# Performance work log

Measured on AMD Instinct MI355X. Metric: run time of the kernel, lower is better.

The kernel has to match this reference:

```python
import jax, jax.numpy as jnp
import numpy as np

B, T = 128, 512          # batch, sequence length (padded game length)
F_IN = 19 * 19           # flattened Go board features
H = 128                  # n_hid
P = 19 * 19 + 1          # policy classes: board points + pass


def setup_inputs() -> dict:
    key = jax.random.key(0)
    ks = jax.random.split(key, 8)
    s = 0.05  # init scale
    return {
        "states": jax.random.normal(ks[0], (B, T, F_IN), jnp.float32),
        "moves": jax.random.randint(ks[1], (B, T), 0, P, jnp.int32),
        "values": jax.random.uniform(ks[2], (B, T), jnp.float32, -1.0, 1.0),
        # LSTM layer 0: concat([x, h]) @ W0 + b0, gates [i, f, g, o]
        "W0": jax.random.normal(ks[3], (F_IN + H, 4 * H), jnp.float32) * s,
        "b0": jnp.zeros((4 * H,), jnp.float32),
        # LSTM layer 1
        "W1": jax.random.normal(ks[4], (H + H, 4 * H), jnp.float32) * s,
        "b1": jnp.zeros((4 * H,), jnp.float32),
        # policy head (size**2 + 1 logits), value head (tanh scalar)
        "Wp": jax.random.normal(ks[5], (H, P), jnp.float32) * s,
        "bp": jnp.zeros((P,), jnp.float32),
        "Wv": jax.random.normal(ks[6], (H, 1), jnp.float32) * s,
        "bv": jnp.zeros((1,), jnp.float32),
    }


def _lstm_cell(h, c, x, W, b):
    # TF LSTMCell: z = [x; h] @ W + b, forget bias 1.0
    z = jnp.concatenate([x, h], axis=-1) @ W + b
    i, f, g, o = jnp.split(z, 4, axis=-1)
    c_new = jax.nn.sigmoid(f + 1.0) * c + jax.nn.sigmoid(i) * jnp.tanh(g)
    h_new = jax.nn.sigmoid(o) * jnp.tanh(c_new)
    return h_new, c_new


def reference(states, moves, values, W0, b0, W1, b1, Wp, bp, Wv, bv):
    b = states.shape[0]
    zeros = jnp.zeros((b, H), states.dtype)

    def step(carry, x_t):
        h0, c0, h1, c1 = carry
        h0, c0 = _lstm_cell(h0, c0, x_t, W0, b0)
        h1, c1 = _lstm_cell(h1, c1, h0, W1, b1)
        return (h0, c0, h1, c1), h1

    _, hs = jax.lax.scan(step, (zeros, zeros, zeros, zeros),
                         jnp.swapaxes(states, 0, 1))  # hs: [T, B, H]
    outputs = jnp.swapaxes(hs, 0, 1)                  # [B, T, H]

    policy_logits = outputs @ Wp + bp                 # [B, T, P]
    winners = jnp.tanh(outputs @ Wv + bv)[..., 0]     # [B, T]

    mask = (values != -9.0).astype(jnp.float32)
    n_mask = mask.sum()

    logp = jax.nn.log_softmax(policy_logits, axis=-1)
    xent = -jnp.take_along_axis(logp, moves[..., None].astype(jnp.int32), axis=-1)[..., 0]
    policy_loss = (mask * xent).sum() / n_mask
    value_loss = (mask * jnp.square(winners - values)).sum() / n_mask
    acc = (moves == jnp.argmax(policy_logits, axis=-1).astype(moves.dtype)).astype(jnp.float32).mean()
    return jnp.stack([policy_loss, value_loss, acc])
```

## Files before the change

kernel.cpp:

```cpp
#include <hip/hip_runtime.h>
#include <hip/hip_bf16.h>
#include <stdint.h>


typedef short v8s __attribute__((ext_vector_type(8)));
typedef float v4f __attribute__((ext_vector_type(4)));
typedef int   v8i __attribute__((ext_vector_type(8)));

#define MFMA_B16(a,b,c) __builtin_amdgcn_mfma_f32_16x16x32_bf16((a),(b),(c),0,0,0)
#define MFMA_MX(a,b,c) \
  __builtin_amdgcn_mfma_scale_f32_16x16x128_f8f6f4((a),(b),(c),0,0,0,0x7F7F7F7F,0,0x7F7F7F7F)

#define NT     512
#define FIN    361
#define KP0    384
#define NPC    362
#define NPP    368

#define OFF_Z    ((size_t)0)
#define OFF_H1   ((size_t)83886080)
#define OFF_W0XT ((size_t)100663296)
#define OFF_WPT  ((size_t)101187584)
#define OFF_B0P  ((size_t)101281792)
#define OFF_BPP  ((size_t)101285888)
#define OFF_ACC  ((size_t)101287936)

static __device__ __forceinline__ short f2b(float f) {
  __hip_bfloat16 h = __float2bfloat16(f);
  union { __hip_bfloat16 h; short s; } cv; cv.h = h; return cv.s;
}
static __device__ __forceinline__ float b2f(unsigned int lo16) {
  union { unsigned u; float f; } cv; cv.u = lo16 << 16; return cv.f;
}
static __device__ __forceinline__ unsigned f2e4m3(float f) {
  union { float f; unsigned u; } cv; cv.f = f;
  unsigned s = (cv.u >> 31) << 7;
  float a = fabsf(f);
  a = fminf(a, 448.f);
  unsigned code;
  if (a >= 0.015625f) {
    union { float f; unsigned u; } m; m.f = a;
    unsigned u = m.u + 0x7FFFF + ((m.u >> 20) & 1);
    code = (u >> 20) - 960;
    if (code > 126u) code = 126u;
  } else {
    code = (unsigned)rintf(a * 512.f);
  }
  return s | code;
}
static __device__ __forceinline__ unsigned f2e4m3_fast(float f) {
#if __has_builtin(__builtin_amdgcn_cvt_pk_fp8_f32)
  return (unsigned)__builtin_amdgcn_cvt_pk_fp8_f32(f, f, 0, false) & 0xffu;
#else
  return f2e4m3(f);
#endif
}

static __device__ __forceinline__ void sync_lds() {
  __builtin_amdgcn_sched_barrier(0);
  asm volatile("s_waitcnt lgkmcnt(0)" ::: "memory");
  __builtin_amdgcn_s_barrier();
  __builtin_amdgcn_sched_barrier(0);
}

__global__ __launch_bounds__(256) void k_conv_weights(
    const float* __restrict__ W0, const float* __restrict__ b0,
    const float* __restrict__ Wp, const float* __restrict__ bp,
    char* __restrict__ ws) {
  int idx = blockIdx.x * 256 + threadIdx.x;
  __hip_bfloat16* W0xT = (__hip_bfloat16*)(ws + OFF_W0XT);
  __hip_bfloat16* WpT  = (__hip_bfloat16*)(ws + OFF_WPT);
  float* b0p = (float*)(ws + OFF_B0P);
  float* bpp = (float*)(ws + OFF_BPP);
  float* acc = (float*)(ws + OFF_ACC);

  if (idx < 196608) {
    int np = idx / 384, k = idx - np * 384;
    int n = (np >> 2) + 128 * (np & 3);
    float v = (k < FIN) ? W0[(size_t)k * 512 + n] : 0.f;
    W0xT[idx] = __float2bfloat16(v);
    return;
  }
  idx -= 196608;
  if (idx < 47104) {
    int p = idx >> 7, k = idx & 127;
    WpT[idx] = __float2bfloat16(p < NPC ? Wp[(size_t)k * NPC + p] : 0.f);
    return;
  }
  idx -= 47104;
  if (idx < 512) {
    int n = (idx >> 2) + 128 * (idx & 3);
    b0p[idx] = b0[n] + (((idx & 3) == 1) ? 1.0f : 0.0f);
    return;
  }
  idx -= 512;
  if (idx < NPP) { bpp[idx] = (idx < NPC) ? bp[idx] : -1e30f; return; }
  idx -= NPP;
  if (idx < 4) { acc[idx] = 0.f; return; }
}

template<int KTOT, bool AF32>
__global__ __launch_bounds__(256) void k_gemm(
    const void* __restrict__ Ap, const __hip_bfloat16* __restrict__ BT,
    const float* __restrict__ bias, __hip_bfloat16* __restrict__ C) {
  __shared__ char sm[65536];
  const int tid = threadIdx.x;
  const int l = tid & 63, wm = tid >> 6;
  const int c = l & 15, lg = l >> 4;
  const int m0 = blockIdx.x * 128;
  const int n0 = blockIdx.y * 128;
  constexpr int NS = KTOT / 64;

  uint4 ra[4], rb[4];
  float fa[32];

  auto LD = [&](int ks) {
#pragma unroll
    for (int i = 0; i < 4; i++) {
      int idx = i * 4096 + tid * 16;
      int row = idx >> 7, colb = idx & 127;
      if constexpr (AF32) {
        int r = m0 + row;
        const float* src = (const float*)Ap + ((size_t)(r & 127) * NT + (r >> 7)) * FIN;
        int kb = ks * 64 + (colb >> 1);
#pragma unroll
        for (int u = 0; u < 8; u++) {
          int kf = kb + u;
          fa[i * 8 + u] = (kf < FIN) ? src[kf] : 0.f;
        }
      } else {
        ra[i] = *(const uint4*)((const char*)Ap + ((size_t)(m0 + row) * KTOT + ks * 64) * 2 + colb);
      }
      rb[i] = *(const uint4*)((const char*)BT + ((size_t)(n0 + row) * KTOT + ks * 64) * 2 + colb);
    }
  };
  auto ST = [&](int bsel) {
#pragma unroll
    for (int i = 0; i < 4; i++) {
      int idx = i * 4096 + tid * 16;
      int row = idx >> 7, colb = idx & 127;
      int sw = colb ^ ((row & 7) << 4);
      if constexpr (AF32) {
        v8s w;
#pragma unroll
        for (int u = 0; u < 8; u++) w[u] = f2b(fa[i * 8 + u]);
        *(v8s*)(sm + bsel * 16384 + row * 128 + sw) = w;
      } else {
        *(uint4*)(sm + bsel * 16384 + row * 128 + sw) = ra[i];
      }
      *(uint4*)(sm + 32768 + bsel * 16384 + row * 128 + sw) = rb[i];
    }
  };

  v4f acc[2][8];
  v4f z4 = {0.f, 0.f, 0.f, 0.f};
#pragma unroll
  for (int mt = 0; mt < 2; mt++)
#pragma unroll
    for (int nt = 0; nt < 8; nt++) acc[mt][nt] = z4;

  LD(0); ST(0);
  __syncthreads();
  for (int ks = 0; ks < NS; ks++) {
    if (ks + 1 < NS) LD(ks + 1);
    const int bsel = ks & 1;
#pragma unroll
    for (int kk = 0; kk < 2; kk++) {
      int bir = kk * 64 + lg * 16;
      v8s af[2];
#pragma unroll
      for (int mt = 0; mt < 2; mt++) {
        int row = wm * 32 + mt * 16 + c;
        af[mt] = *(v8s*)(sm + bsel * 16384 + row * 128 + (bir ^ ((row & 7) << 4)));
      }
#pragma unroll
      for (int nt = 0; nt < 8; nt++) {
        int n = nt * 16 + c;
        v8s bf = *(v8s*)(sm + 32768 + bsel * 16384 + n * 128 + (bir ^ ((n & 7) << 4)));
#pragma unroll
        for (int mt = 0; mt < 2; mt++) acc[mt][nt] = MFMA_B16(af[mt], bf, acc[mt][nt]);
      }
    }
    if (ks + 1 < NS) ST((ks + 1) & 1);
    __syncthreads();
  }

#pragma unroll
  for (int mt = 0; mt < 2; mt++)
#pragma unroll
    for (int nt = 0; nt < 8; nt++) {
      int colp = n0 + nt * 16 + c;
      float bs = bias[colp];
#pragma unroll
      for (int j = 0; j < 4; j++) {
        int row = m0 + wm * 32 + mt * 16 + lg * 4 + j;
        C[(size_t)row * 512 + colp] = __float2bfloat16(acc[mt][nt][j] + bs);
      }
    }
}

__global__ __launch_bounds__(1024, 4) void k_scan12(
    const __hip_bfloat16* __restrict__ Z, const float* __restrict__ W0f,
    const float* __restrict__ W1f, const float* __restrict__ b1,
    __hip_bfloat16* __restrict__ h1out) {
  __shared__ char sm[8192];
  const int tid = threadIdx.x;
  const int l = tid & 63, wv = tid >> 6;
  const int c = l & 15, lg = l >> 4;
  const int role = wv >> 3, rw = wv & 7;
  const int B0 = blockIdx.x * 4;
  const int m_ = 16 * rw + c;
  const int row = 4 * lg;
  v4f z4 = {0.f, 0.f, 0.f, 0.f};
  const int wf8 = row * 128 + (((m_ >> 3) ^ row) << 3) + (m_ & 7);

  for (int e = tid * 4; e < 8192; e += 1024 * 4) *(int*)(sm + e) = 0;

  auto AFRAG = [&](int base) -> v8i {
    union { unsigned long long q[4]; v8i v; } u;
#pragma unroll
    for (int t = 0; t < 4; t++)
      u.q[t] = *(const unsigned long long*)(
          sm + base + c * 128 + ((((lg * 4 + t) ^ c) & 15) << 3));
    return u.v;
  };

  if (role == 0) {
    v8i breg[4];
#pragma unroll
    for (int g = 0; g < 4; g++) {
      int n = g * 128 + m_;
      union { unsigned long long q[4]; v8i v; } u;
#pragma unroll
      for (int t = 0; t < 4; t++) {
        unsigned long long w = 0ull;
#pragma unroll
        for (int j = 0; j < 8; j++) {
          int k = lg * 32 + t * 8 + j;
          w |= (unsigned long long)f2e4m3(W0f[(size_t)(FIN + k) * 512 + n]) << (8 * j);
        }
        u.q[t] = w;
      }
      breg[g] = u.v;
    }

    uint2 zA, zB, zC;
    auto ZLD = [&](int t) -> uint2 {
      return *(const uint2*)(Z + ((size_t)t * 128 + B0 + lg) * 512 + m_ * 4);
    };
    zA = ZLD(0); zB = ZLD(1);
    float cst = 0.f;
    __syncthreads();

    for (int s = 0; s < NT; s++) {
      v8i av = AFRAG(((s + 1) & 1) * 2048);
      v4f acc[4];
#pragma unroll
      for (int g = 0; g < 4; g++) acc[g] = z4;
#pragma unroll
      for (int g = 0; g < 4; g++) acc[g] = MFMA_MX(av, breg[g], acc[g]);
      if (s + 2 < NT) zC = ZLD(s + 2);

      float xi = acc[0][0] + b2f(zA.x & 0xffffu);
      float xf = acc[1][0] + b2f(zA.x >> 16);
      float xg = acc[2][0] + b2f(zA.y & 0xffffu);
      float xo = acc[3][0] + b2f(zA.y >> 16);
      float ei = __expf(-xi);
      float ef = __expf(-xf);
      float eg = __expf(2.f * xg);
      float eo = __expf(-xo);
      float cn = cst * __builtin_amdgcn_rcpf(1.f + ef)
               + (eg - 1.f) * __builtin_amdgcn_rcpf((1.f + ei) * (eg + 1.f));
      cst = cn;
      float ec = __expf(2.f * cn);
      float hv = (ec - 1.f) * __builtin_amdgcn_rcpf((1.f + eo) * (ec + 1.f));
      *(unsigned char*)(sm + (s & 1) * 2048 + wf8) = (unsigned char)f2e4m3_fast(hv);
      zA = zB; zB = zC;
      sync_lds();
    }
    sync_lds();
  } else {
    v8i bregH[4], bregX[4];
#pragma unroll
    for (int g = 0; g < 4; g++) {
      int n = g * 128 + m_;
      union { unsigned long long q[4]; v8i v; } uh, ux;
#pragma unroll
      for (int t = 0; t < 4; t++) {
        unsigned long long wh = 0ull, wx = 0ull;
#pragma unroll
        for (int j = 0; j < 8; j++) {
          int k = lg * 32 + t * 8 + j;
          wh |= (unsigned long long)f2e4m3(W1f[(size_t)(128 + k) * 512 + n]) << (8 * j);
          wx |= (unsigned long long)f2e4m3(W1f[(size_t)k * 512 + n]) << (8 * j);
        }
        uh.q[t] = wh; ux.q[t] = wx;
      }
      bregH[g] = uh.v; bregX[g] = ux.v;
    }
    float bq[4];
#pragma unroll
    for (int g = 0; g < 4; g++)
      bq[g] = b1[g * 128 + m_] + ((g == 1) ? 1.0f : 0.0f);
    float cst = 0.f;
    __syncthreads();
    sync_lds();

    for (int s = 1; s <= NT; s++) {
      v8i ah = AFRAG(4096 + (s & 1) * 2048);
      v8i ax = AFRAG(((s + 1) & 1) * 2048);
      v4f acc[4];
#pragma unroll
      for (int g = 0; g < 4; g++) acc[g] = (v4f){bq[g], bq[g], bq[g], bq[g]};
#pragma unroll
      for (int g = 0; g < 4; g++) acc[g] = MFMA_MX(ah, bregH[g], acc[g]);
#pragma unroll
      for (int g = 0; g < 4; g++) acc[g] = MFMA_MX(ax, bregX[g], acc[g]);

      float xi = acc[0][0], xf = acc[1][0], xg = acc[2][0], xo = acc[3][0];
      float ei = __expf(-xi);
      float ef = __expf(-xf);
      float eg = __expf(2.f * xg);
      float eo = __expf(-xo);
      float cn = cst * __builtin_amdgcn_rcpf(1.f + ef)
               + (eg - 1.f) * __builtin_amdgcn_rcpf((1.f + ei) * (eg + 1.f));
      cst = cn;
      float ec = __expf(2.f * cn);
      float hv = (ec - 1.f) * __builtin_amdgcn_rcpf((1.f + eo) * (ec + 1.f));
      *(unsigned char*)(sm + 4096 + ((s + 1) & 1) * 2048 + wf8) =
          (unsigned char)f2e4m3_fast(hv);
      union { short s; __hip_bfloat16 h; } cv; cv.s = f2b(hv);
      h1out[((size_t)(s - 1) * 128 + B0 + lg) * 128 + m_] = cv.h;
      sync_lds();
    }
  }
}

__global__ __launch_bounds__(256) void k_heads(
    const __hip_bfloat16* __restrict__ Hh, const __hip_bfloat16* __restrict__ WpT,
    const float* __restrict__ bpp, const float* __restrict__ Wv,
    const float* __restrict__ bv, const int* __restrict__ moves,
    const float* __restrict__ values, float* __restrict__ accum) {
  __shared__ char sm[110592];
  const int tid = threadIdx.x;
  const int l = tid & 63, wm = tid >> 6;
  const int c = l & 15, lg = l >> 4;
  const int r0 = blockIdx.x * 64;

#pragma unroll
  for (int i = 0; i < 4; i++) {
    int idx = i * 4096 + tid * 16;
    int row = idx >> 8, colb = idx & 255;
    uint4 v = *(const uint4*)((const char*)Hh + (size_t)r0 * 256 + idx);
    *(uint4*)(sm + row * 256 + (colb ^ ((row & 7) << 4))) = v;
  }
#pragma unroll
  for (int i = 0; i < 23; i++) {
    int idx = i * 4096 + tid * 16;
    int row = idx >> 8, colb = idx & 255;
    uint4 v = *(const uint4*)((const char*)WpT + idx);
    *(uint4*)(sm + 16384 + row * 256 + (colb ^ ((row & 7) << 4))) = v;
  }
  __syncthreads();

  v4f acc[23];
  v4f z4 = {0.f, 0.f, 0.f, 0.f};
#pragma unroll
  for (int q = 0; q < 23; q++) acc[q] = z4;
#pragma unroll
  for (int kk = 0; kk < 4; kk++) {
    int bir = kk * 64 + lg * 16;
    int ar = wm * 16 + c;
    v8s a = *(v8s*)(sm + ar * 256 + (bir ^ ((ar & 7) << 4)));
#pragma unroll
    for (int q = 0; q < 23; q++) {
      int n = q * 16 + c;
      v8s b = *(v8s*)(sm + 16384 + n * 256 + (bir ^ ((n & 7) << 4)));
      acc[q] = MFMA_B16(a, b, acc[q]);
    }
  }
  float bq[23];
#pragma unroll
  for (int q = 0; q < 23; q++) bq[q] = bpp[q * 16 + c];

  float tp = 0.f, tv = 0.f, ta = 0.f, tn = 0.f;
#pragma unroll
  for (int j = 0; j < 4; j++) {
    int rloc = lg * 4 + j;
    int r = r0 + wm * 16 + rloc;
    int t = r >> 7, b = r & 127;
    int mv = moves[(size_t)b * NT + t];
    float val = values[(size_t)b * NT + t];
    float msk = (val != -9.0f) ? 1.f : 0.f;

    float pmax = -3.0e38f;
#pragma unroll
    for (int q = 0; q < 23; q++) pmax = fmaxf(pmax, acc[q][j] + bq[q]);
#pragma unroll
    for (int d = 1; d < 16; d <<= 1) pmax = fmaxf(pmax, __shfl_xor(pmax, d, 64));
    float ps = 0.f;
#pragma unroll
    for (int q = 0; q < 23; q++) ps += __expf((acc[q][j] + bq[q]) - pmax);
#pragma unroll
    for (int d = 1; d < 16; d <<= 1) ps += __shfl_xor(ps, d, 64);
    float lse = pmax + __logf(ps);

    int qm = mv >> 4, cm = mv & 15;
    float mlv = 0.f;
#pragma unroll
    for (int q = 0; q < 23; q++) if (q == qm) mlv = acc[q][j] + bq[q];
    mlv = __shfl(mlv, (l & 48) + cm, 64);
    float xent = lse - mlv;

    float amx = -3.0e38f; int aix = 0;
#pragma unroll
    for (int q = 0; q < 23; q++) {
      float v = acc[q][j] + bq[q];
      if (v > amx) { amx = v; aix = q * 16 + c; }
    }
#pragma unroll
    for (int d = 1; d < 16; d <<= 1) {
      float ov = __shfl_xor(amx, d, 64);
      int oi = __shfl_xor(aix, d, 64);
      if (ov > amx || (ov == amx && oi < aix)) { amx = ov; aix = oi; }
    }

    float pd = 0.f;
    int vrow = wm * 16 + rloc;
#pragma unroll
    for (int i = 0; i < 8; i++) {
      int k = c * 8 + i;
      short hv = *(short*)(sm + vrow * 256 + ((k * 2) ^ ((vrow & 7) << 4)));
      pd += b2f((unsigned short)hv) * Wv[k];
    }
#pragma unroll
    for (int d = 1; d < 16; d <<= 1) pd += __shfl_xor(pd, d, 64);
    float eo = __expf(2.f * (pd + bv[0]));
    float win = (eo - 1.f) * __builtin_amdgcn_rcpf(eo + 1.f);
    float dv = win - val;

    if (c == 0) {
      tp += msk * xent;
      tv += msk * dv * dv;
      ta += (aix == mv) ? 1.f : 0.f;
      tn += msk;
    }
  }
  tp += __shfl_xor(tp, 16, 64); tp += __shfl_xor(tp, 32, 64);
  tv += __shfl_xor(tv, 16, 64); tv += __shfl_xor(tv, 32, 64);
  ta += __shfl_xor(ta, 16, 64); ta += __shfl_xor(ta, 32, 64);
  tn += __shfl_xor(tn, 16, 64); tn += __shfl_xor(tn, 32, 64);
  if (l == 0) {
    atomicAdd(accum + 0, tp);
    atomicAdd(accum + 1, tv);
    atomicAdd(accum + 2, ta);
    atomicAdd(accum + 3, tn);
  }
}

__global__ void k_final(const float* __restrict__ accum, float* __restrict__ out) {
  if (threadIdx.x == 0) {
    float nm = accum[3];
    out[0] = accum[0] / nm;
    out[1] = accum[1] / nm;
    out[2] = accum[2] / 65536.0f;
  }
}

extern "C" void kernel_launch(void* const* d_in, const int* in_sizes, int n_in,
                              void* d_out, int out_size, void* d_ws, size_t ws_size,
                              hipStream_t stream) {
  (void)in_sizes; (void)n_in; (void)out_size; (void)ws_size;
  const float* states = (const float*)d_in[0];
  const int*   moves  = (const int*)d_in[1];
  const float* values = (const float*)d_in[2];
  const float* W0 = (const float*)d_in[3];
  const float* b0 = (const float*)d_in[4];
  const float* W1 = (const float*)d_in[5];
  const float* b1 = (const float*)d_in[6];
  const float* Wp = (const float*)d_in[7];
  const float* bp = (const float*)d_in[8];
  const float* Wv = (const float*)d_in[9];
  const float* bv = (const float*)d_in[10];
  char* ws = (char*)d_ws;

  __hip_bfloat16* zbuf = (__hip_bfloat16*)(ws + OFF_Z);
  __hip_bfloat16* h1   = (__hip_bfloat16*)(ws + OFF_H1);
  __hip_bfloat16* W0xT = (__hip_bfloat16*)(ws + OFF_W0XT);
  __hip_bfloat16* WpT  = (__hip_bfloat16*)(ws + OFF_WPT);
  float* b0p = (float*)(ws + OFF_B0P);
  float* bpp = (float*)(ws + OFF_BPP);
  float* acc = (float*)(ws + OFF_ACC);

  k_conv_weights<<<956, 256, 0, stream>>>(W0, b0, Wp, bp, ws);
  k_gemm<KP0, true><<<dim3(512, 4), 256, 0, stream>>>(states, W0xT, b0p, zbuf);
  k_scan12<<<32, 1024, 0, stream>>>(zbuf, W0, W1, b1, h1);
  k_heads<<<1024, 256, 0, stream>>>(h1, WpT, bpp, Wv, bv, moves, values, acc);
  k_final<<<1, 1, 0, stream>>>(acc, (float*)d_out);
}
```

Baseline: 829.5 us.

## Halve scan block to 512 threads, two hidden columns per lane

The recurrent LSTM scan kernel now runs with 8 waves instead of 16. Each wave handles two 16-column tiles, so each lane keeps two sets of fp8 weight fragments and two cell states. The intent is to cut the cost of the per-timestep workgroup barrier across fewer waves and to reuse each loaded A fragment for twice as many MFMAs. The cell math is also restructured to use one reciprocal instead of two. The cost is more registers and more serial work per wave on the critical recurrence path.

```diff
diff --git a/kernel.cpp b/kernel.cpp
--- a/kernel.cpp
+++ b/kernel.cpp
@@ -1,5 +1,9 @@
 #include <hip/hip_runtime.h>
 #include <hip/hip_bf16.h>
+#if __has_include(<hip/hip_fp8.h>)
+#include <hip/hip_fp8.h>
+#define HAVE_HIP_FP8 1
+#endif
 #include <stdint.h>
 
 
@@ -29,8 +33,11 @@
   __hip_bfloat16 h = __float2bfloat16(f);
   union { __hip_bfloat16 h; short s; } cv; cv.h = h; return cv.s;
 }
+static __device__ __forceinline__ float u2f(unsigned int bits) {
+  union { unsigned u; float f; } cv; cv.u = bits; return cv.f;
+}
 static __device__ __forceinline__ float b2f(unsigned int lo16) {
-  union { unsigned u; float f; } cv; cv.u = lo16 << 16; return cv.f;
+  return u2f(lo16 << 16);
 }
 static __device__ __forceinline__ unsigned f2e4m3(float f) {
   union { float f; unsigned u; } cv; cv.f = f;
@@ -48,9 +55,12 @@
   }
   return s | code;
 }
-static __device__ __forceinline__ unsigned f2e4m3_fast(float f) {
+static __device__ __forceinline__ unsigned cvt8(float f) {
 #if __has_builtin(__builtin_amdgcn_cvt_pk_fp8_f32)
   return (unsigned)__builtin_amdgcn_cvt_pk_fp8_f32(f, f, 0, false) & 0xffu;
+#elif defined(HAVE_HIP_FP8)
+  __hip_fp8_e4m3 h(f);
+  return (unsigned)h.__x;
 #else
   return f2e4m3(f);
 #endif
@@ -199,7 +209,7 @@
     }
 }
 
-__global__ __launch_bounds__(1024, 4) void k_scan12(
+__global__ __launch_bounds__(512, 2) void k_scan12(
     const __hip_bfloat16* __restrict__ Z, const float* __restrict__ W0f,
     const float* __restrict__ W1f, const float* __restrict__ b1,
     __hip_bfloat16* __restrict__ h1out) {
@@ -207,14 +217,14 @@
   const int tid = threadIdx.x;
   const int l = tid & 63, wv = tid >> 6;
   const int c = l & 15, lg = l >> 4;
-  const int role = wv >> 3, rw = wv & 7;
+  const int role = wv >> 2, rw = wv & 3;
   const int B0 = blockIdx.x * 4;
-  const int m_ = 16 * rw + c;
+  const int m1 = 16 * rw + c, m2 = m1 + 64;
   const int row = 4 * lg;
-  v4f z4 = {0.f, 0.f, 0.f, 0.f};
-  const int wf8 = row * 128 + (((m_ >> 3) ^ row) << 3) + (m_ & 7);
-
-  for (int e = tid * 4; e < 8192; e += 1024 * 4) *(int*)(sm + e) = 0;
+  const int wf81 = row * 128 + (((m1 >> 3) ^ row) << 3) + (m1 & 7);
+  const int wf82 = row * 128 + (((m2 >> 3) ^ row) << 3) + (m2 & 7);
+
+  for (int e = tid * 4; e < 8192; e += 512 * 4) *(int*)(sm + e) = 0;
 
   auto AFRAG = [&](int base) -> v8i {
     union { unsigned long long q[4]; v8i v; } u;
@@ -225,112 +235,137 @@
     return u.v;
   };
 
+  auto CELL = [&](float xi, float xf, float xg, float xo, float& cst) -> float {
+    float ei = __expf(-xi);
+    float ef = __expf(-xf);
+    float eg = __expf(2.f * xg);
+    float eo = __expf(-xo);
+    float t1 = 1.f + ef, t2 = 1.f + ei, t3 = eg + 1.f;
+    float p = t2 * t3;
+    float num = cst * p + (eg - 1.f) * t1;
+    float cn = num * __builtin_amdgcn_rcpf(t1 * p);
+    cst = cn;
+    float ec = __expf(2.f * cn);
+    return (ec - 1.f) * __builtin_amdgcn_rcpf((1.f + eo) * (ec + 1.f));
+  };
+
   if (role == 0) {
-    v8i breg[4];
-#pragma unroll
-    for (int g = 0; g < 4; g++) {
-      int n = g * 128 + m_;
-      union { unsigned long long q[4]; v8i v; } u;
-#pragma unroll
-      for (int t = 0; t < 4; t++) {
-        unsigned long long w = 0ull;
-#pragma unroll
-        for (int j = 0; j < 8; j++) {
-          int k = lg * 32 + t * 8 + j;
-          w |= (unsigned long long)f2e4m3(W0f[(size_t)(FIN + k) * 512 + n]) << (8 * j);
+    v8i breg[4][2];
+#pragma unroll
+    for (int g = 0; g < 4; g++)
+#pragma unroll
+      for (int u = 0; u < 2; u++) {
+        int n = g * 128 + (u ? m2 : m1);
+        union { unsigned long long q[4]; v8i v; } w;
+#pragma unroll
+        for (int t = 0; t < 4; t++) {
+          unsigned long long x = 0ull;
+#pragma unroll
+          for (int j = 0; j < 8; j++) {
+            int k = lg * 32 + t * 8 + j;
+            x |= (unsigned long long)f2e4m3(W0f[(size_t)(FIN + k) * 512 + n]) << (8 * j);
+          }
+          w.q[t] = x;
         }
-        u.q[t] = w;
-      }
-      breg[g] = u.v;
-    }
-
-    uint2 zA, zB, zC;
-    auto ZLD = [&](int t) -> uint2 {
-      return *(const uint2*)(Z + ((size_t)t * 128 + B0 + lg) * 512 + m_ * 4);
+        breg[g][u] = w.v;
+      }
+
+    uint2 zA[2], zB[2], zC[2];
+    auto ZLD = [&](int t, uint2* dst) {
+      dst[0] = *(const uint2*)(Z + ((size_t)t * 128 + B0 + lg) * 512 + m1 * 4);
+      dst[1] = *(const uint2*)(Z + ((size_t)t * 128 + B0 + lg) * 512 + m2 * 4);
     };
-    zA = ZLD(0); zB = ZLD(1);
-    float cst = 0.f;
+    ZLD(0, zA); ZLD(1, zB);
+    float cst1 = 0.f, cst2 = 0.f;
     __syncthreads();
 
     for (int s = 0; s < NT; s++) {
       v8i av = AFRAG(((s + 1) & 1) * 2048);
-      v4f acc[4];
-#pragma unroll
-      for (int g = 0; g < 4; g++) acc[g] = z4;
-#pragma unroll
-      for (int g = 0; g < 4; g++) acc[g] = MFMA_MX(av, breg[g], acc[g]);
-      if (s + 2 < NT) zC = ZLD(s + 2);
-
-      float xi = acc[0][0] + b2f(zA.x & 0xffffu);
-      float xf = acc[1][0] + b2f(zA.x >> 16);
-      float xg = acc[2][0] + b2f(zA.y & 0xffffu);
-      float xo = acc[3][0] + b2f(zA.y >> 16);
-      float ei = __expf(-xi);
-      float ef = __expf(-xf);
-      float eg = __expf(2.f * xg);
-      float eo = __expf(-xo);
-      float cn = cst * __builtin_amdgcn_rcpf(1.f + ef)
-               + (eg - 1.f) * __builtin_amdgcn_rcpf((1.f + ei) * (eg + 1.f));
-      cst = cn;
-      float ec = __expf(2.f * cn);
-      float hv = (ec - 1.f) * __builtin_amdgcn_rcpf((1.f + eo) * (ec + 1.f));
-      *(unsigned char*)(sm + (s & 1) * 2048 + wf8) = (unsigned char)f2e4m3_fast(hv);
-      zA = zB; zB = zC;
+      v4f acc[4][2];
+#pragma unroll
+      for (int g = 0; g < 4; g++)
+#pragma unroll
+        for (int u = 0; u < 2; u++) acc[g][u] = (v4f){0.f, 0.f, 0.f, 0.f};
+#pragma unroll
+      for (int g = 0; g < 4; g++)
+#pragma unroll
+        for (int u = 0; u < 2; u++)
+          acc[g][u] = MFMA_MX(av, breg[g][u], acc[g][u]);
+      if (s + 2 < NT) ZLD(s + 2, zC);
+
+      float h1v = CELL(acc[0][0][0] + u2f(zA[0].x << 16),
+                       acc[1][0][0] + u2f(zA[0].x & 0xffff0000u),
+                       acc[2][0][0] + u2f(zA[0].y << 16),
+                       acc[3][0][0] + u2f(zA[0].y & 0xffff0000u), cst1);
+      float h2v = CELL(acc[0][1][0] + u2f(zA[1].x << 16),
+                       acc[1][1][0] + u2f(zA[1].x & 0xffff0000u),
+                       acc[2][1][0] + u2f(zA[1].y << 16),
+                       acc[3][1][0] + u2f(zA[1].y & 0xffff0000u), cst2);
+      *(unsigned char*)(sm + (s & 1) * 2048 + wf81) = (unsigned char)cvt8(h1v);
+      *(unsigned char*)(sm + (s & 1) * 2048 + wf82) = (unsigned char)cvt8(h2v);
+      zA[0] = zB[0]; zA[1] = zB[1]; zB[0] = zC[0]; zB[1] = zC[1];
       sync_lds();
     }
     sync_lds();
   } else {
-    v8i bregH[4], bregX[4];
+    v8i bregH[4][2], bregX[4][2];
+#pragma unroll
+    for (int g = 0; g < 4; g++)
+#pragma unroll
+      for (int u = 0; u < 2; u++) {
+        int n = g * 128 + (u ? m2 : m1);
+        union { unsigned long long q[4]; v8i v; } wh, wx;
+#pragma unroll
+        for (int t = 0; t < 4; t++) {
+          unsigned long long xh = 0ull, xx = 0ull;
+#pragma unroll
+          for (int j = 0; j < 8; j++) {
+            int k = lg * 32 + t * 8 + j;
+            xh |= (unsigned long long)f2e4m3(W1f[(size_t)(128 + k) * 512 + n]) << (8 * j);
+            xx |= (unsigned long long)f2e4m3(W1f[(size_t)k * 512 + n]) << (8 * j);
+          }
+          wh.q[t] = xh; wx.q[t] = xx;
+        }
+        bregH[g][u] = wh.v; bregX[g][u] = wx.v;
+      }
+    float bq[4][2];
 #pragma unroll
     for (int g = 0; g < 4; g++) {
-      int n = g * 128 + m_;
-      union { unsigned long long q[4]; v8i v; } uh, ux;
-#pragma unroll
-      for (int t = 0; t < 4; t++) {
-        unsigned long long wh = 0ull, wx = 0ull;
-#pragma unroll
-        for (int j = 0; j < 8; j++) {
-          int k = lg * 32 + t * 8 + j;
-          wh |= (unsigned long long)f2e4m3(W1f[(size_t)(128 + k) * 512 + n]) << (8 * j);
-          wx |= (unsigned long long)f2e4m3(W1f[(size_t)k * 512 + n]) << (8 * j);
-        }
-        uh.q[t] = wh; ux.q[t] = wx;
-      }
-      bregH[g] = uh.v; bregX[g] = ux.v;
-    }
-    float bq[4];
-#pragma unroll
-    for (int g = 0; g < 4; g++)
-      bq[g] = b1[g * 128 + m_] + ((g == 1) ? 1.0f : 0.0f);
-    float cst = 0.f;
+      bq[g][0] = b1[g * 128 + m1] + ((g == 1) ? 1.0f : 0.0f);
+      bq[g][1] = b1[g * 128 + m2] + ((g == 1) ? 1.0f : 0.0f);
+    }
+    float cst1 = 0.f, cst2 = 0.f;
     __syncthreads();
     sync_lds();
 
     for (int s = 1; s <= NT; s++) {
       v8i ah = AFRAG(4096 + (s & 1) * 2048);
       v8i ax = AFRAG(((s + 1) & 1) * 2048);
-      v4f acc[4];
-#pragma unroll
-      for (int g = 0; g < 4; g++) acc[g] = (v4f){bq[g], bq[g], bq[g], bq[g]};
-#pragma unroll
-      for (int g = 0; g < 4; g++) acc[g] = MFMA_MX(ah, bregH[g], acc[g]);
-#pragma unroll
-      for (int g = 0; g < 4; g++) acc[g] = MFMA_MX(ax, bregX[g], acc[g]);
-
-      float xi = acc[0][0], xf = acc[1][0], xg = acc[2][0], xo = acc[3][0];
-      float ei = __expf(-xi);
-      float ef = __expf(-xf);
-      float eg = __expf(2.f * xg);
-      float eo = __expf(-xo);
-      float cn = cst * __builtin_amdgcn_rcpf(1.f + ef)
-               + (eg - 1.f) * __builtin_amdgcn_rcpf((1.f + ei) * (eg + 1.f));
-      cst = cn;
-      float ec = __expf(2.f * cn);
-      float hv = (ec - 1.f) * __builtin_amdgcn_rcpf((1.f + eo) * (ec + 1.f));
-      *(unsigned char*)(sm + 4096 + ((s + 1) & 1) * 2048 + wf8) =
-          (unsigned char)f2e4m3_fast(hv);
-      union { short s; __hip_bfloat16 h; } cv; cv.s = f2b(hv);
-      h1out[((size_t)(s - 1) * 128 + B0 + lg) * 128 + m_] = cv.h;
+      v4f acc[4][2];
+#pragma unroll
+      for (int g = 0; g < 4; g++)
+#pragma unroll
+        for (int u = 0; u < 2; u++)
+          acc[g][u] = (v4f){bq[g][u], bq[g][u], bq[g][u], bq[g][u]};
+#pragma unroll
+      for (int g = 0; g < 4; g++)
+#pragma unroll
+        for (int u = 0; u < 2; u++)
+          acc[g][u] = MFMA_MX(ah, bregH[g][u], acc[g][u]);
+#pragma unroll
+      for (int g = 0; g < 4; g++)
+#pragma unroll
+        for (int u = 0; u < 2; u++)
+          acc[g][u] = MFMA_MX(ax, bregX[g][u], acc[g][u]);
+
+      float h1v = CELL(acc[0][0][0], acc[1][0][0], acc[2][0][0], acc[3][0][0], cst1);
+      float h2v = CELL(acc[0][1][0], acc[1][1][0], acc[2][1][0], acc[3][1][0], cst2);
+      *(unsigned char*)(sm + 4096 + ((s + 1) & 1) * 2048 + wf81) = (unsigned char)cvt8(h1v);
+      *(unsigned char*)(sm + 4096 + ((s + 1) & 1) * 2048 + wf82) = (unsigned char)cvt8(h2v);
+      union { short s; __hip_bfloat16 h; } cv1, cv2;
+      cv1.s = f2b(h1v); cv2.s = f2b(h2v);
+      h1out[((size_t)(s - 1) * 128 + B0 + lg) * 128 + m1] = cv1.h;
+      h1out[((size_t)(s - 1) * 128 + B0 + lg) * 128 + m2] = cv2.h;
       sync_lds();
     }
   }
@@ -494,7 +529,7 @@
 
   k_conv_weights<<<956, 256, 0, stream>>>(W0, b0, Wp, bp, ws);
   k_gemm<KP0, true><<<dim3(512, 4), 256, 0, stream>>>(states, W0xT, b0p, zbuf);
-  k_scan12<<<32, 1024, 0, stream>>>(zbuf, W0, W1, b1, h1);
+  k_scan12<<<32, 512, 0, stream>>>(zbuf, W0, W1, b1, h1);
   k_heads<<<1024, 256, 0, stream>>>(h1, WpT, bpp, Wv, bv, moves, values, acc);
   k_final<<<1, 1, 0, stream>>>(acc, (float*)d_out);
 }
```

Result: slower. 1.002 ms (+20.8%).
